# Optimization experiments

Measured on AMD Instinct MI355X. Metric: run time of the kernel, lower is better.

## Reference

```python
import jax, jax.numpy as jnp
import numpy as np

N = 10000
E = 320000
D = 256


def setup_inputs() -> dict:
    key = jax.random.key(0)
    ks = jax.random.split(key, 10)
    s = 1.0 / np.sqrt(D)
    return {
        "x0": jax.random.normal(ks[0], (N, D), jnp.float32),
        "edge_index": jax.random.randint(ks[1], (2, E), 0, N, jnp.int32),
        "W1": jax.random.normal(ks[2], (D, D), jnp.float32) * s,
        "b1": jax.random.normal(ks[3], (D,), jnp.float32) * s,
        "W2": jax.random.normal(ks[4], (D, D), jnp.float32) * s,
        "b2": jax.random.normal(ks[5], (D,), jnp.float32) * s,
        "wa1": jax.random.normal(ks[6], (D,), jnp.float32) * s,
        "ba1": jax.random.normal(ks[7], (1,), jnp.float32) * s,
        "wa2": jax.random.normal(ks[8], (D,), jnp.float32) * s,
        "ba2": jax.random.normal(ks[9], (1,), jnp.float32) * s,
    }


def reference(x0, edge_index, W1, b1, W2, b2, wa1, ba1, wa2, ba2):
    n = x0.shape[0]
    leaky = lambda v: jax.nn.leaky_relu(v, 0.2)
    x0_i = leaky(x0 @ W1 + b1)                      # [N, D]
    x0_j = leaky(x0 @ W2 + b2)                      # [N, D]
    a1 = x0_i @ wa1 + ba1[0]                        # [N]
    a2 = x0_j @ wa2 + ba2[0]                        # [N]
    row, col = edge_index[0], edge_index[1]
    # sigmoid(a_1 + a_2.T)[row, col] without the dense N x N intermediate
    att = jax.nn.sigmoid(a1[row] + a2[col])         # [E]
    msg = att[:, None] * x0_j[col]                  # [E, D]
    out = jax.ops.segment_sum(msg, row, num_segments=n)  # sparse.mm(attention, x0_j)
    return out + x0
```

## Files before the change

kernel.cpp:

```cpp
#include <hip/hip_runtime.h>
#include <math.h>

#define D 256
#define CAP 128
#define APAD 264

typedef float f32x4 __attribute__((ext_vector_type(4)));
typedef short s16x8 __attribute__((ext_vector_type(8)));
typedef unsigned short u16x8 __attribute__((ext_vector_type(8)));

static __device__ __forceinline__ unsigned short f2bf(float x) {
    union { float f; unsigned u; } v; v.f = x;
    unsigned r = v.u + 0x7fff + ((v.u >> 16) & 1);
    return (unsigned short)(r >> 16);
}

__global__ __launch_bounds__(256) void k_init(
    const float* __restrict__ W1, const float* __restrict__ W2,
    unsigned short* __restrict__ wt, int* __restrict__ curp, int n)
{
    const int i = blockIdx.x * 256 + threadIdx.x;
    if (i < 2 * D * D) {
        int k = i >> 9;
        int j = i & 511;
        float v = (j < D) ? W1[(size_t)k * D + j] : W2[(size_t)k * D + (j - D)];
        wt[(size_t)j * D + k] = f2bf(v);
    }
    if (i < n) curp[(size_t)i << 5] = 0;
}

__global__ __launch_bounds__(256) void k_mfma_rank(
    const float* __restrict__ x0, const unsigned short* __restrict__ wt,
    const float* __restrict__ b1, const float* __restrict__ b2,
    const float* __restrict__ wa1, const float* __restrict__ wa2,
    const float* __restrict__ ba1, const float* __restrict__ ba2,
    const int* __restrict__ rows, const int* __restrict__ cols,
    int* __restrict__ curp, unsigned short* __restrict__ perm,
    unsigned char* __restrict__ x0j8, float* __restrict__ a1,
    float2* __restrict__ a2s, int n, int e, int nrb)
{
    __shared__ unsigned short Atile[32][APAD];
    __shared__ float part[4][32];
    __shared__ float pmx[2][32];
    __shared__ float sscale[32];
    const int t = threadIdx.x;

    if ((int)blockIdx.x < nrb) {
        const int i0 = (blockIdx.x * 256 + t) * 8;
        if (i0 + 7 < e) {
            int4 ra = *(const int4*)&rows[i0];
            int4 rb4 = *(const int4*)&rows[i0 + 4];
            int4 ca = *(const int4*)&cols[i0];
            int4 cb4 = *(const int4*)&cols[i0 + 4];
            int s0 = atomicAdd(&curp[(size_t)ra.x << 5], 1);
            int s1 = atomicAdd(&curp[(size_t)ra.y << 5], 1);
            int s2 = atomicAdd(&curp[(size_t)ra.z << 5], 1);
            int s3 = atomicAdd(&curp[(size_t)ra.w << 5], 1);
            int s4 = atomicAdd(&curp[(size_t)rb4.x << 5], 1);
            int s5 = atomicAdd(&curp[(size_t)rb4.y << 5], 1);
            int s6 = atomicAdd(&curp[(size_t)rb4.z << 5], 1);
            int s7 = atomicAdd(&curp[(size_t)rb4.w << 5], 1);
            if (s0 < CAP) perm[(size_t)ra.x * CAP + s0] = (unsigned short)ca.x;
            if (s1 < CAP) perm[(size_t)ra.y * CAP + s1] = (unsigned short)ca.y;
            if (s2 < CAP) perm[(size_t)ra.z * CAP + s2] = (unsigned short)ca.z;
            if (s3 < CAP) perm[(size_t)ra.w * CAP + s3] = (unsigned short)ca.w;
            if (s4 < CAP) perm[(size_t)rb4.x * CAP + s4] = (unsigned short)cb4.x;
            if (s5 < CAP) perm[(size_t)rb4.y * CAP + s5] = (unsigned short)cb4.y;
            if (s6 < CAP) perm[(size_t)rb4.z * CAP + s6] = (unsigned short)cb4.z;
            if (s7 < CAP) perm[(size_t)rb4.w * CAP + s7] = (unsigned short)cb4.w;
        } else {
            for (int i = i0; i < e; ++i) {
                int r = rows[i];
                int slot = atomicAdd(&curp[(size_t)r << 5], 1);
                if (slot < CAP) perm[(size_t)r * CAP + slot] = (unsigned short)cols[i];
            }
        }
        return;
    }

    const int lane = t & 63, w = t >> 6;
    const int rb = (blockIdx.x - nrb) * 32;
    const int lr = lane & 15;
    const int kg = lane >> 4;

    for (int s = t; s < 32 * 32; s += 256) {
        const int row = s >> 5, seg = s & 31;
        int gr = rb + row; if (gr >= n) gr = n - 1;
        f32x4 v0 = *(const f32x4*)&x0[(size_t)gr * D + seg * 8];
        f32x4 v1 = *(const f32x4*)&x0[(size_t)gr * D + seg * 8 + 4];
        u16x8 o;
        o[0] = f2bf(v0.x); o[1] = f2bf(v0.y); o[2] = f2bf(v0.z); o[3] = f2bf(v0.w);
        o[4] = f2bf(v1.x); o[5] = f2bf(v1.y); o[6] = f2bf(v1.z); o[7] = f2bf(v1.w);
        *(u16x8*)&Atile[row][seg * 8] = o;
    }
    __syncthreads();

    const int cb = w * 128;
    f32x4 acc[2][8] = {};

    #pragma unroll
    for (int ks = 0; ks < 8; ++ks) {
        const int k0 = ks * 32 + kg * 8;
        s16x8 af[2];
        af[0] = *(const s16x8*)&Atile[lr][k0];
        af[1] = *(const s16x8*)&Atile[16 + lr][k0];
        s16x8 bfr[8];
        #pragma unroll
        for (int cf = 0; cf < 8; ++cf)
            bfr[cf] = *(const s16x8*)&wt[(size_t)(cb + cf * 16 + lr) * D + k0];
        #pragma unroll
        for (int rf = 0; rf < 2; ++rf)
            #pragma unroll
            for (int cf = 0; cf < 8; ++cf)
                acc[rf][cf] = __builtin_amdgcn_mfma_f32_16x16x32_bf16(
                    af[rf], bfr[cf], acc[rf][cf], 0, 0, 0);
    }

    const bool isW2 = (w >= 2);
    const float* wav  = isW2 ? wa2 : wa1;
    const float* bias = isW2 ? b2  : b1;
    const int crel = cb - (isW2 ? D : 0);

    float bvv[8], wvv[8];
    #pragma unroll
    for (int cf = 0; cf < 8; ++cf) {
        bvv[cf] = bias[crel + cf * 16 + lr];
        wvv[cf] = wav[crel + cf * 16 + lr];
    }

    float rs[2][4] = {};
    float mx[2][4] = {};
    #pragma unroll
    for (int rf = 0; rf < 2; ++rf)
        #pragma unroll
        for (int cf = 0; cf < 8; ++cf)
            #pragma unroll
            for (int r = 0; r < 4; ++r) {
                float v = acc[rf][cf][r] + bvv[cf];
                v = (v > 0.0f) ? v : 0.2f * v;
                rs[rf][r] += v * wvv[cf];
                mx[rf][r] = fmaxf(mx[rf][r], fabsf(v));
            }

    #pragma unroll
    for (int rf = 0; rf < 2; ++rf)
        #pragma unroll
        for (int r = 0; r < 4; ++r) {
            float s = rs[rf][r], m = mx[rf][r];
            #pragma unroll
            for (int o = 1; o < 16; o <<= 1) {
                s += __shfl_xor(s, o, 64);
                m = fmaxf(m, __shfl_xor(m, o, 64));
            }
            if (lr == 0) {
                const int ri = rf * 16 + kg * 4 + r;
                part[w][ri] = s;
                if (isW2) pmx[w - 2][ri] = m;
            }
        }
    __syncthreads();
    if (t < 32) {
        const int row = rb + t;
        float smax = fmaxf(fmaxf(pmx[0][t], pmx[1][t]), 1e-20f);
        float sc = smax * (1.0f / 127.0f);
        sscale[t] = sc;
        if (row < n) {
            a1[row] = part[0][t] + part[1][t] + ba1[0] + ba2[0];
            float2 av; av.x = part[2][t] + part[3][t]; av.y = sc;
            a2s[row] = av;
        }
    }
    __syncthreads();

    if (isW2) {
        #pragma unroll
        for (int rf = 0; rf < 2; ++rf)
            #pragma unroll
            for (int r = 0; r < 4; ++r) {
                const int ri = rf * 16 + kg * 4 + r;
                const int row = rb + ri;
                if (row >= n) continue;
                const float inv_s = 1.0f / sscale[ri];
                #pragma unroll
                for (int cf = 0; cf < 8; ++cf) {
                    const int col = crel + cf * 16 + lr;
                    float v = acc[rf][cf][r] + bvv[cf];
                    v = (v > 0.0f) ? v : 0.2f * v;
                    int qv = (int)rintf(v * inv_s) + 128;
                    qv = (qv < 0) ? 0 : ((qv > 255) ? 255 : qv);
                    x0j8[(size_t)row * D + col] = (unsigned char)qv;
                }
            }
    }
}

__global__ __launch_bounds__(256) void k_agg(
    const unsigned char* __restrict__ x0j8, const float* __restrict__ x0,
    const float* __restrict__ a1, const float2* __restrict__ a2s,
    const int* __restrict__ curp, const unsigned short* __restrict__ perm,
    float* __restrict__ out, int n)
{
    __shared__ unsigned short scol[4][CAP + 4];
    __shared__ float satt[4][CAP + 4];

    const int w = threadIdx.x >> 6, lane = threadIdx.x & 63;
    const int q = lane >> 4, hl = lane & 15;
    const int row = blockIdx.x * 4 + w;

    int deg = 0;
    f32x4 res;
    if (row < n) {
        deg = curp[(size_t)row << 5];
        if (deg > CAP) deg = CAP;
        const size_t pbase = (size_t)row * CAP;
        const float a1r = a1[row];
        res = *(const f32x4*)&x0[(size_t)row * D + hl * 16 + q * 4];

        for (int i = lane; i < deg; i += 64) {
            int c = perm[pbase + i];
            scol[w][i] = (unsigned short)c;
            float2 p = a2s[c];
            float att = 1.0f / (1.0f + __expf(-(a1r + p.x)));
            satt[w][i] = att * p.y;
        }
        if (lane < 4) {
            scol[w][deg + lane] = 0;
            satt[w][deg + lane] = 0.0f;
        }
    }
    __syncthreads();
    if (row >= n) return;

    const int degp = (deg + 3) & ~3;

    float acc[16];
    #pragma unroll
    for (int k = 0; k < 16; ++k) acc[k] = 0.0f;
    float corr = 0.0f;

    #pragma unroll 2
    for (int j = 0; j < degp; j += 4) {
        const int idx = j + q;
        const float as = satt[w][idx];
        const int   c  = scol[w][idx];
        uint4 v = *(const uint4*)&x0j8[(size_t)c * D + hl * 16];
        corr += as;
        acc[0]  += as * (float)( v.x        & 255);
        acc[1]  += as * (float)((v.x >>  8) & 255);
        acc[2]  += as * (float)((v.x >> 16) & 255);
        acc[3]  += as * (float)( v.x >> 24);
        acc[4]  += as * (float)( v.y        & 255);
        acc[5]  += as * (float)((v.y >>  8) & 255);
        acc[6]  += as * (float)((v.y >> 16) & 255);
        acc[7]  += as * (float)( v.y >> 24);
        acc[8]  += as * (float)( v.z        & 255);
        acc[9]  += as * (float)((v.z >>  8) & 255);
        acc[10] += as * (float)((v.z >> 16) & 255);
        acc[11] += as * (float)( v.z >> 24);
        acc[12] += as * (float)( v.w        & 255);
        acc[13] += as * (float)((v.w >>  8) & 255);
        acc[14] += as * (float)((v.w >> 16) & 255);
        acc[15] += as * (float)( v.w >> 24);
    }

    #pragma unroll
    for (int k = 0; k < 16; ++k) acc[k] += __shfl_xor(acc[k], 16, 64);
    corr += __shfl_xor(corr, 16, 64);
    #pragma unroll
    for (int k = 0; k < 16; ++k) acc[k] += __shfl_xor(acc[k], 32, 64);
    corr += __shfl_xor(corr, 32, 64);

    const float bias128 = 128.0f * corr;

    float s0, s1, s2, s3;
    if      (q == 0) { s0 = acc[0];  s1 = acc[1];  s2 = acc[2];  s3 = acc[3];  }
    else if (q == 1) { s0 = acc[4];  s1 = acc[5];  s2 = acc[6];  s3 = acc[7];  }
    else if (q == 2) { s0 = acc[8];  s1 = acc[9];  s2 = acc[10]; s3 = acc[11]; }
    else             { s0 = acc[12]; s1 = acc[13]; s2 = acc[14]; s3 = acc[15]; }

    const int col = hl * 16 + q * 4;
    f32x4 o;
    o.x = res.x + s0 - bias128;
    o.y = res.y + s1 - bias128;
    o.z = res.z + s2 - bias128;
    o.w = res.w + s3 - bias128;
    *(f32x4*)&out[(size_t)row * D + col] = o;
}

extern "C" void kernel_launch(void* const* d_in, const int* in_sizes, int n_in,
                              void* d_out, int out_size, void* d_ws, size_t ws_size,
                              hipStream_t stream)
{
    const float* x0  = (const float*)d_in[0];
    const int*   ei  = (const int*)d_in[1];
    const float* W1  = (const float*)d_in[2];
    const float* b1  = (const float*)d_in[3];
    const float* W2  = (const float*)d_in[4];
    const float* b2  = (const float*)d_in[5];
    const float* wa1 = (const float*)d_in[6];
    const float* ba1 = (const float*)d_in[7];
    const float* wa2 = (const float*)d_in[8];
    const float* ba2 = (const float*)d_in[9];
    float* out = (float*)d_out;

    const int n = in_sizes[0] / D;
    const int e = in_sizes[1] / 2;
    const int* rows = ei;
    const int* cols = ei + e;

    char* ws = (char*)d_ws;
    unsigned short* wt   = (unsigned short*)ws;
    unsigned char*  x0j8 = (unsigned char*)(wt + (size_t)2 * D * D);
    float*  a1   = (float*)(x0j8 + (size_t)n * D);
    float2* a2s  = (float2*)(a1 + n);
    int*    curp = (int*)(a2s + n);
    unsigned short* perm = (unsigned short*)(curp + (size_t)n * 32);

    const int ithreads = 2 * D * D;
    k_init<<<(ithreads + 255) / 256, 256, 0, stream>>>(W1, W2, wt, curp, n);
    const int gx = (n + 31) / 32;
    const int nrb = (e / 8 + 255) / 256;
    k_mfma_rank<<<nrb + gx, 256, 0, stream>>>(x0, wt, b1, b2, wa1, wa2,
                                              ba1, ba2, rows, cols, curp, perm,
                                              x0j8, a1, a2s, n, e, nrb);
    k_agg<<<(n + 3) / 4, 256, 0, stream>>>(x0j8, x0, a1, a2s, curp, perm, out, n);
}
```

Measured before the change: 53.64 us.

## Split GEMM blocks across four column quarters and pre-convert x0 to bf16

The fused GEMM kernel previously had one block compute all 512 output columns for 32 rows, staging x0 as bf16 in shared memory. Now k_init converts all of x0 to bf16 up front, and each 32-row tile is split into four blocks of 128 columns each, with every wave handling 32 columns and reading A fragments straight from global memory. Partial attention logits go to a per-row 4-slot array, and int8 quantization scales become per half of x0_j, so the aggregation kernel keeps two scaled attention arrays and picks one by column segment. This gives four times as many GEMM blocks and less register pressure, at the cost of an extra pass over x0, redundant A reads across blocks, and a slightly different quantization granularity.

```diff
diff --git a/kernel.cpp b/kernel.cpp
--- a/kernel.cpp
+++ b/kernel.cpp
@@ -3,7 +3,6 @@
 
 #define D 256
 #define CAP 128
-#define APAD 264
 
 typedef float f32x4 __attribute__((ext_vector_type(4)));
 typedef short s16x8 __attribute__((ext_vector_type(8)));
@@ -16,10 +15,18 @@
 }
 
 __global__ __launch_bounds__(256) void k_init(
-    const float* __restrict__ W1, const float* __restrict__ W2,
+    const float* __restrict__ x0, const float* __restrict__ W1,
+    const float* __restrict__ W2, unsigned short* __restrict__ xb,
     unsigned short* __restrict__ wt, int* __restrict__ curp, int n)
 {
     const int i = blockIdx.x * 256 + threadIdx.x;
+    const int nx4 = n * D / 4;
+    if (i < nx4) {
+        f32x4 v = *(const f32x4*)&x0[(size_t)i * 4];
+        ushort4 o;
+        o.x = f2bf(v.x); o.y = f2bf(v.y); o.z = f2bf(v.z); o.w = f2bf(v.w);
+        *(ushort4*)&xb[(size_t)i * 4] = o;
+    }
     if (i < 2 * D * D) {
         int k = i >> 9;
         int j = i & 511;
@@ -30,18 +37,16 @@
 }
 
 __global__ __launch_bounds__(256) void k_mfma_rank(
-    const float* __restrict__ x0, const unsigned short* __restrict__ wt,
+    const unsigned short* __restrict__ xb, const unsigned short* __restrict__ wt,
     const float* __restrict__ b1, const float* __restrict__ b2,
     const float* __restrict__ wa1, const float* __restrict__ wa2,
-    const float* __restrict__ ba1, const float* __restrict__ ba2,
     const int* __restrict__ rows, const int* __restrict__ cols,
     int* __restrict__ curp, unsigned short* __restrict__ perm,
-    unsigned char* __restrict__ x0j8, float* __restrict__ a1,
-    float2* __restrict__ a2s, int n, int e, int nrb)
+    unsigned char* __restrict__ x0j8, float* __restrict__ pa,
+    float* __restrict__ sA, float* __restrict__ sB, int n, int e, int nrb)
 {
-    __shared__ unsigned short Atile[32][APAD];
     __shared__ float part[4][32];
-    __shared__ float pmx[2][32];
+    __shared__ float pmx[4][32];
     __shared__ float sscale[32];
     const int t = threadIdx.x;
 
@@ -79,51 +84,45 @@
     }
 
     const int lane = t & 63, w = t >> 6;
-    const int rb = (blockIdx.x - nrb) * 32;
+    const int bid2 = blockIdx.x - nrb;
+    const int bx = bid2 >> 2, by = bid2 & 3;
+    const int rb = bx * 32;
+    const int cb = by * 128 + w * 32;
     const int lr = lane & 15;
     const int kg = lane >> 4;
 
-    for (int s = t; s < 32 * 32; s += 256) {
-        const int row = s >> 5, seg = s & 31;
-        int gr = rb + row; if (gr >= n) gr = n - 1;
-        f32x4 v0 = *(const f32x4*)&x0[(size_t)gr * D + seg * 8];
-        f32x4 v1 = *(const f32x4*)&x0[(size_t)gr * D + seg * 8 + 4];
-        u16x8 o;
-        o[0] = f2bf(v0.x); o[1] = f2bf(v0.y); o[2] = f2bf(v0.z); o[3] = f2bf(v0.w);
-        o[4] = f2bf(v1.x); o[5] = f2bf(v1.y); o[6] = f2bf(v1.z); o[7] = f2bf(v1.w);
-        *(u16x8*)&Atile[row][seg * 8] = o;
-    }
-    __syncthreads();
-
-    const int cb = w * 128;
-    f32x4 acc[2][8] = {};
+    f32x4 acc[2][2] = {};
 
     #pragma unroll
     for (int ks = 0; ks < 8; ++ks) {
         const int k0 = ks * 32 + kg * 8;
-        s16x8 af[2];
-        af[0] = *(const s16x8*)&Atile[lr][k0];
-        af[1] = *(const s16x8*)&Atile[16 + lr][k0];
-        s16x8 bfr[8];
-        #pragma unroll
-        for (int cf = 0; cf < 8; ++cf)
-            bfr[cf] = *(const s16x8*)&wt[(size_t)(cb + cf * 16 + lr) * D + k0];
+        s16x8 af[2], bfr[2];
+        #pragma unroll
+        for (int rf = 0; rf < 2; ++rf) {
+            int row = rb + rf * 16 + lr; if (row >= n) row = n - 1;
+            af[rf] = *(const s16x8*)&xb[(size_t)row * D + k0];
+        }
+        #pragma unroll
+        for (int cf = 0; cf < 2; ++cf) {
+            int col = cb + cf * 16 + lr;
+            bfr[cf] = *(const s16x8*)&wt[(size_t)col * D + k0];
+        }
         #pragma unroll
         for (int rf = 0; rf < 2; ++rf)
             #pragma unroll
-            for (int cf = 0; cf < 8; ++cf)
+            for (int cf = 0; cf < 2; ++cf)
                 acc[rf][cf] = __builtin_amdgcn_mfma_f32_16x16x32_bf16(
                     af[rf], bfr[cf], acc[rf][cf], 0, 0, 0);
     }
 
-    const bool isW2 = (w >= 2);
+    const bool isW2 = (by >= 2);
     const float* wav  = isW2 ? wa2 : wa1;
     const float* bias = isW2 ? b2  : b1;
     const int crel = cb - (isW2 ? D : 0);
 
-    float bvv[8], wvv[8];
-    #pragma unroll
-    for (int cf = 0; cf < 8; ++cf) {
+    float bvv[2], wvv[2];
+    #pragma unroll
+    for (int cf = 0; cf < 2; ++cf) {
         bvv[cf] = bias[crel + cf * 16 + lr];
         wvv[cf] = wav[crel + cf * 16 + lr];
     }
@@ -133,7 +132,7 @@
     #pragma unroll
     for (int rf = 0; rf < 2; ++rf)
         #pragma unroll
-        for (int cf = 0; cf < 8; ++cf)
+        for (int cf = 0; cf < 2; ++cf)
             #pragma unroll
             for (int r = 0; r < 4; ++r) {
                 float v = acc[rf][cf][r] + bvv[cf];
@@ -155,19 +154,22 @@
             if (lr == 0) {
                 const int ri = rf * 16 + kg * 4 + r;
                 part[w][ri] = s;
-                if (isW2) pmx[w - 2][ri] = m;
+                pmx[w][ri] = m;
             }
         }
     __syncthreads();
     if (t < 32) {
         const int row = rb + t;
-        float smax = fmaxf(fmaxf(pmx[0][t], pmx[1][t]), 1e-20f);
+        float smax = fmaxf(fmaxf(pmx[0][t], pmx[1][t]),
+                           fmaxf(pmx[2][t], pmx[3][t]));
+        smax = fmaxf(smax, 1e-20f);
         float sc = smax * (1.0f / 127.0f);
         sscale[t] = sc;
         if (row < n) {
-            a1[row] = part[0][t] + part[1][t] + ba1[0] + ba2[0];
-            float2 av; av.x = part[2][t] + part[3][t]; av.y = sc;
-            a2s[row] = av;
+            pa[((size_t)row << 2) + by] =
+                part[0][t] + part[1][t] + part[2][t] + part[3][t];
+            if (by == 2) sA[row] = sc;
+            else if (by == 3) sB[row] = sc;
         }
     }
     __syncthreads();
@@ -182,7 +184,7 @@
                 if (row >= n) continue;
                 const float inv_s = 1.0f / sscale[ri];
                 #pragma unroll
-                for (int cf = 0; cf < 8; ++cf) {
+                for (int cf = 0; cf < 2; ++cf) {
                     const int col = crel + cf * 16 + lr;
                     float v = acc[rf][cf][r] + bvv[cf];
                     v = (v > 0.0f) ? v : 0.2f * v;
@@ -196,12 +198,14 @@
 
 __global__ __launch_bounds__(256) void k_agg(
     const unsigned char* __restrict__ x0j8, const float* __restrict__ x0,
-    const float* __restrict__ a1, const float2* __restrict__ a2s,
-    const int* __restrict__ curp, const unsigned short* __restrict__ perm,
-    float* __restrict__ out, int n)
+    const float* __restrict__ pa, const float* __restrict__ sA,
+    const float* __restrict__ sB, const float* __restrict__ ba1,
+    const float* __restrict__ ba2, const int* __restrict__ curp,
+    const unsigned short* __restrict__ perm, float* __restrict__ out, int n)
 {
     __shared__ unsigned short scol[4][CAP + 4];
-    __shared__ float satt[4][CAP + 4];
+    __shared__ float sscA[4][CAP + 4];
+    __shared__ float sscB[4][CAP + 4];
 
     const int w = threadIdx.x >> 6, lane = threadIdx.x & 63;
     const int q = lane >> 4, hl = lane & 15;
@@ -213,25 +217,29 @@
         deg = curp[(size_t)row << 5];
         if (deg > CAP) deg = CAP;
         const size_t pbase = (size_t)row * CAP;
-        const float a1r = a1[row];
+        const float a1r = pa[(size_t)row * 4] + pa[(size_t)row * 4 + 1]
+                        + ba1[0] + ba2[0];
         res = *(const f32x4*)&x0[(size_t)row * D + hl * 16 + q * 4];
 
         for (int i = lane; i < deg; i += 64) {
             int c = perm[pbase + i];
             scol[w][i] = (unsigned short)c;
-            float2 p = a2s[c];
-            float att = 1.0f / (1.0f + __expf(-(a1r + p.x)));
-            satt[w][i] = att * p.y;
+            float2 a2p = *(const float2*)&pa[((size_t)c << 2) + 2];
+            float att = 1.0f / (1.0f + __expf(-(a1r + a2p.x + a2p.y)));
+            sscA[w][i] = att * sA[c];
+            sscB[w][i] = att * sB[c];
         }
         if (lane < 4) {
             scol[w][deg + lane] = 0;
-            satt[w][deg + lane] = 0.0f;
+            sscA[w][deg + lane] = 0.0f;
+            sscB[w][deg + lane] = 0.0f;
         }
     }
     __syncthreads();
     if (row >= n) return;
 
     const int degp = (deg + 3) & ~3;
+    const bool segA = (hl < 8);
 
     float acc[16];
     #pragma unroll
@@ -241,7 +249,7 @@
     #pragma unroll 2
     for (int j = 0; j < degp; j += 4) {
         const int idx = j + q;
-        const float as = satt[w][idx];
+        const float as = segA ? sscA[w][idx] : sscB[w][idx];
         const int   c  = scol[w][idx];
         uint4 v = *(const uint4*)&x0j8[(size_t)c * D + hl * 16];
         corr += as;
@@ -310,18 +318,22 @@
 
     char* ws = (char*)d_ws;
     unsigned short* wt   = (unsigned short*)ws;
-    unsigned char*  x0j8 = (unsigned char*)(wt + (size_t)2 * D * D);
-    float*  a1   = (float*)(x0j8 + (size_t)n * D);
-    float2* a2s  = (float2*)(a1 + n);
-    int*    curp = (int*)(a2s + n);
+    unsigned short* xb   = wt + (size_t)2 * D * D;
+    unsigned char*  x0j8 = (unsigned char*)(xb + (size_t)n * D);
+    float* pa   = (float*)(x0j8 + (size_t)n * D);
+    float* sA   = pa + (size_t)4 * n;
+    float* sB   = sA + n;
+    int*   curp = (int*)(sB + n);
     unsigned short* perm = (unsigned short*)(curp + (size_t)n * 32);
 
-    const int ithreads = 2 * D * D;
-    k_init<<<(ithreads + 255) / 256, 256, 0, stream>>>(W1, W2, wt, curp, n);
-    const int gx = (n + 31) / 32;
+    const int ithreads = n * D / 4;
+    k_init<<<(ithreads + 255) / 256, 256, 0, stream>>>(x0, W1, W2, xb, wt,
+                                                       curp, n);
+    const int gx4 = ((n + 31) / 32) * 4;
     const int nrb = (e / 8 + 255) / 256;
-    k_mfma_rank<<<nrb + gx, 256, 0, stream>>>(x0, wt, b1, b2, wa1, wa2,
-                                              ba1, ba2, rows, cols, curp, perm,
-                                              x0j8, a1, a2s, n, e, nrb);
-    k_agg<<<(n + 3) / 4, 256, 0, stream>>>(x0j8, x0, a1, a2s, curp, perm, out, n);
-}
+    k_mfma_rank<<<nrb + gx4, 256, 0, stream>>>(xb, wt, b1, b2, wa1, wa2,
+                                               rows, cols, curp, perm,
+                                               x0j8, pa, sA, sB, n, e, nrb);
+    k_agg<<<(n + 3) / 4, 256, 0, stream>>>(x0j8, x0, pa, sA, sB, ba1, ba2,
+                                           curp, perm, out, n);
+}
```

Result: slower. 63.46 us (+18.3%).
